# Performance work log

Measured on AMD Instinct MI355X. Metric: run time of the kernel, lower is better.

## Reference

```python
import jax, jax.numpy as jnp
import numpy as np


def setup_inputs() -> dict:
    key = jax.random.key(0)
    k1, k2, k3, k4 = jax.random.split(key, 4)
    B, T, M, Din, Dout = 32, 24, 512, 64, 64
    x = jax.random.normal(k1, (B, T, M, Din), dtype=jnp.float32)
    adj = jax.random.uniform(k2, (M, M), dtype=jnp.float32)
    adj = adj / jnp.sum(adj, axis=-1, keepdims=True)  # row-normalized adjacency
    route_weights = jax.random.normal(k3, (M, Din, Dout), dtype=jnp.float32) * 0.05
    route_bias = jax.random.normal(k4, (M, 1, Dout), dtype=jnp.float32) * 0.05
    return {"x": x, "adj": adj, "route_weights": route_weights, "route_bias": route_bias}


def reference(x, adj, route_weights, route_bias):
    B, T, M, _ = x.shape
    xf = x.reshape(B * T, M, -1)                      # [BT, M, Din]
    # shared adjacency applied across all B*T graphs: one contraction instead of
    # a broadcast bmm
    h = jnp.einsum('mn,bnd->bmd', adj, xf)            # [BT, M, Din]
    # per-node (per-route) weight transform + per-route bias
    h = jnp.einsum('bmd,mdl->bml', h, route_weights)  # [BT, M, Dout]
    h = h + route_bias[:, 0, :][None, :, :]           # bias per route m
    return h.reshape(B, T, M, -1)
```

## Files before the change

kernel.cpp:

```cpp
#include <hip/hip_runtime.h>
#include <stdint.h>

typedef short bf16x8 __attribute__((ext_vector_type(8)));
typedef unsigned short u16x8 __attribute__((ext_vector_type(8)));
typedef float f32x4 __attribute__((ext_vector_type(4)));
typedef float f32x8 __attribute__((ext_vector_type(8)));

constexpr int BT_TOT = 768;
constexpr int M_N    = 512;
constexpr int DD     = 64;
constexpr int WROW   = 72;

__device__ __forceinline__ unsigned short f2bf(float f) {
  unsigned u = __builtin_bit_cast(unsigned, f);
  u += 0x7fffu + ((u >> 16) & 1u);
  return (unsigned short)(u >> 16);
}
__device__ __forceinline__ unsigned pk2(float a, float b) {
  return (unsigned)f2bf(a) | ((unsigned)f2bf(b) << 16);
}

__global__ __launch_bounds__(256)
void prep_adj(const float* __restrict__ adjg, unsigned short* __restrict__ wsadj) {
  int i = (blockIdx.x * 256 + threadIdx.x) * 8;
  f32x8 a = *(const f32x8*)(adjg + i);
  u16x8 r;
  #pragma unroll
  for (int j = 0; j < 8; ++j) r[j] = f2bf(a[j]);
  *(u16x8*)(wsadj + i) = r;
}

template<bool WS>
__global__ __launch_bounds__(512, 2)
void gconv_h(const float* __restrict__ xg,
             const float* __restrict__ adjf,
             const unsigned short* __restrict__ adjb,
             char* __restrict__ hout)
{
  __shared__ char lds[2][32768];

  const int wid  = blockIdx.x;
  const int xcd  = wid & 7;
  const int slot = wid >> 3;
  const int mb   = slot & 3;
  const int btg  = xcd + 8 * (slot >> 2);
  const int bt0  = btg * 2;

  const int tid  = threadIdx.x;
  const int lane = tid & 63;
  const int wv   = tid >> 6;
  const int l15  = lane & 15;
  const int gg   = lane >> 4;
  const int c4   = lane & 15;
  const int wb   = wv & 1;
  const int wm   = wv >> 1;

  const int mlo  = tid >> 3;
  const int oct  = (tid & 7) ^ (mlo & 7);

  f32x4 xv[4];
  u16x8 ab[2];
  f32x8 af_[2];

  auto load_adj = [&](int c) {
    const size_t e0 = (size_t)(mb*128 + mlo     ) * M_N + c*64 + oct*8;
    const size_t e1 = (size_t)(mb*128 + mlo + 64) * M_N + c*64 + oct*8;
    if (WS) { ab[0] = *(const u16x8*)(adjb + e0); ab[1] = *(const u16x8*)(adjb + e1); }
    else    { af_[0] = *(const f32x8*)(adjf + e0); af_[1] = *(const f32x8*)(adjf + e1); }
  };
  auto load_x = [&](int c) {
    #pragma unroll
    for (int s = 0; s < 4; ++s) {
      const int n4 = s*4 + wm;
      xv[s] = *(const f32x4*)(xg + ((size_t)(bt0 + wb) * M_N + c*64 + n4*4 + gg) * DD + c4*4);
    }
  };
  auto write_stage = [&](int c) {
    char* buf = &lds[c & 1][0];
    if (WS) {
      *(u16x8*)(buf + tid*16)        = ab[0];
      *(u16x8*)(buf + 8192 + tid*16) = ab[1];
    } else {
      u16x8 r0, r1;
      #pragma unroll
      for (int j = 0; j < 8; ++j) { r0[j] = f2bf(af_[0][j]); r1[j] = f2bf(af_[1][j]); }
      *(u16x8*)(buf + tid*16)        = r0;
      *(u16x8*)(buf + 8192 + tid*16) = r1;
    }
    char* xt = buf + 16384 + wb*8192;
    const int d = c4*4 + gg;
    #pragma unroll
    for (int s = 0; s < 4; ++s) {
      const int n4 = s*4 + wm;
      unsigned u0 = pk2(xv[s].x, xv[s].y);
      unsigned u1 = pk2(xv[s].z, xv[s].w);
      unsigned t0 = __shfl_xor(u0, 32);
      unsigned t1 = __shfl_xor(u1, 32);
      unsigned v0 = (gg & 2) ? t1 : u0;
      unsigned v1 = (gg & 2) ? u1 : t0;
      unsigned s0 = __shfl_xor(v0, 16);
      unsigned s1 = __shfl_xor(v1, 16);
      unsigned F0 = (gg & 1) ? ((s0 >> 16) | (v0 & 0xFFFF0000u))
                             : ((v0 & 0xFFFFu) | (s0 << 16));
      unsigned F1 = (gg & 1) ? ((s1 >> 16) | (v1 & 0xFFFF0000u))
                             : ((v1 & 0xFFFFu) | (s1 << 16));
      uint2 o2; o2.x = F0; o2.y = F1;
      *(uint2*)(xt + d*128 + (((n4 >> 1) ^ (d & 7)) * 16) + (n4 & 1)*8) = o2;
    }
  };

  f32x4 acc[2][4];
  #pragma unroll
  for (int mt = 0; mt < 2; ++mt)
    #pragma unroll
    for (int dt = 0; dt < 4; ++dt) acc[mt][dt] = f32x4{0.f,0.f,0.f,0.f};

  load_adj(0); load_x(0);

  #pragma unroll 2
  for (int c = 0; c < 8; ++c) {
    write_stage(c);
    __syncthreads();
    if (c < 7) { load_adj(c+1); load_x(c+1); }
    {
      const char* buf  = &lds[c & 1][0];
      const char* adjL = buf;
      const char* xt   = buf + 16384 + wb*8192;
      #pragma unroll
      for (int kl = 0; kl < 2; ++kl) {
        const int sw = ((kl*4 + gg) ^ (l15 & 7)) * 16;
        bf16x8 afr[2], bfx[4];
        #pragma unroll
        for (int mt = 0; mt < 2; ++mt)
          afr[mt] = __builtin_bit_cast(bf16x8,
              *(const u16x8*)(adjL + (wm*32 + mt*16 + l15)*128 + sw));
        #pragma unroll
        for (int dt = 0; dt < 4; ++dt)
          bfx[dt] = __builtin_bit_cast(bf16x8,
              *(const u16x8*)(xt + (dt*16 + l15)*128 + sw));
        #pragma unroll
        for (int mt = 0; mt < 2; ++mt)
          #pragma unroll
          for (int dt = 0; dt < 4; ++dt)
            acc[mt][dt] = __builtin_amdgcn_mfma_f32_16x16x32_bf16(afr[mt], bfx[dt],
                                                                  acc[mt][dt], 0,0,0);
      }
    }
  }

  const int bt = bt0 + wb;
  #pragma unroll
  for (int mt = 0; mt < 2; ++mt)
    #pragma unroll
    for (int dt = 0; dt < 4; ++dt)
      #pragma unroll
      for (int r = 0; r < 4; ++r) {
        int m = mb*128 + wm*32 + mt*16 + gg*4 + r;
        int d = dt*16 + l15;
        *(unsigned short*)(hout + ((size_t)bt*M_N + m)*256 + 2*d)
            = f2bf(acc[mt][dt][r]);
      }
}

__global__ __launch_bounds__(256, 4)
void route_mm(const char* __restrict__ hin,
              const float* __restrict__ wgt,
              const float* __restrict__ bias,
              float* __restrict__ outg)
{
  __shared__ unsigned short wb[128 * WROW];

  const int m0    = blockIdx.x * 2;
  const int btblk = blockIdx.y * 64;
  const int tid   = threadIdx.x;
  const int lane  = tid & 63;
  const int wv    = tid >> 6;
  const int l15   = lane & 15;
  const int gg    = lane >> 4;
  const int dp    = tid & 31;
  const int lo    = tid >> 5;

  { const float* q = wgt + ((size_t)m0*64 + dp*2)*64 + lo*8;
    f32x8 w0 = *(const f32x8*)q;          f32x8 w1 = *(const f32x8*)(q+64);
    f32x8 w2 = *(const f32x8*)(q+4096);   f32x8 w3 = *(const f32x8*)(q+4160);
    #pragma unroll
    for (int e = 0; e < 8; ++e) {
      int lrow = lo*8 + e;
      unsigned v0 = pk2(w0[e], w1[e]);
      unsigned v1 = pk2(w2[e], w3[e]);
      *(unsigned*)(wb + lrow*WROW + dp*2)        = v0;
      *(unsigned*)(wb + (64 + lrow)*WROW + dp*2) = v1;
    }
  }
  __syncthreads();

  const int btw0 = btblk + wv*16;

  #pragma unroll
  for (int mm = 0; mm < 2; ++mm) {
    const int m = m0 + mm;
    bf16x8 afr[2];
    #pragma unroll
    for (int ks = 0; ks < 2; ++ks) {
      const char* hp = hin + ((size_t)(btw0 + l15)*M_N + m)*256 + ks*64 + gg*16;
      afr[ks] = __builtin_bit_cast(bf16x8, *(const u16x8*)hp);
    }
    f32x4 acc[4];
    #pragma unroll
    for (int lt = 0; lt < 4; ++lt) acc[lt] = f32x4{0.f,0.f,0.f,0.f};
    #pragma unroll
    for (int lt = 0; lt < 4; ++lt)
      #pragma unroll
      for (int ks = 0; ks < 2; ++ks) {
        bf16x8 bfr = __builtin_bit_cast(bf16x8,
            *(const u16x8*)(wb + (mm*64 + lt*16 + l15)*WROW + ks*32 + gg*8));
        acc[lt] = __builtin_amdgcn_mfma_f32_16x16x32_bf16(afr[ks], bfr, acc[lt], 0,0,0);
      }
    #pragma unroll
    for (int lt = 0; lt < 4; ++lt) {
      float bv = bias[m*64 + lt*16 + l15];
      #pragma unroll
      for (int r = 0; r < 4; ++r) {
        size_t row = (size_t)(btw0 + gg*4 + r)*M_N + m;
        outg[row*64 + lt*16 + l15] = acc[lt][r] + bv;
      }
    }
  }
}

extern "C" void kernel_launch(void* const* d_in, const int* in_sizes, int n_in,
                              void* d_out, int out_size, void* d_ws, size_t ws_size,
                              hipStream_t stream) {
  const float* xg   = (const float*)d_in[0];
  const float* adjg = (const float*)d_in[1];
  const float* wgt  = (const float*)d_in[2];
  const float* bg   = (const float*)d_in[3];

  const size_t adj_bf_bytes = (size_t)M_N * M_N * 2;
  if (ws_size >= adj_bf_bytes) {
    unsigned short* wsadj = (unsigned short*)d_ws;
    prep_adj<<<dim3(M_N * M_N / (256 * 8)), dim3(256), 0, stream>>>(adjg, wsadj);
    gconv_h<true><<<dim3(1536), dim3(512), 0, stream>>>(
        xg, adjg, wsadj, (char*)d_out);
  } else {
    gconv_h<false><<<dim3(1536), dim3(512), 0, stream>>>(
        xg, adjg, nullptr, (char*)d_out);
  }
  route_mm<<<dim3(M_N/2, BT_TOT/64), dim3(256), 0, stream>>>(
      (const char*)d_out, wgt, bg, (float*)d_out);
}
```

Measured before the change: 99.45 us.

## Load adjacency fragments directly from global and shrink gconv blocks to one BT

The graph-conv kernel no longer stages adjacency tiles in shared memory. Each wave loads its bf16 A-fragments straight from global memory (the bf16 copy is expected to stay in L2), and only the x tile is double-buffered in LDS. Blocks now handle a single bt with 256 threads, so twice as many blocks launch and each uses less LDS, which allows more blocks per CU. The trade-off is that adjacency is no longer shared through LDS across the two bt slices, so global/L2 traffic for it doubles, and its load latency is exposed inside the loop.

```diff
diff --git a/kernel.cpp b/kernel.cpp
--- a/kernel.cpp
+++ b/kernel.cpp
@@ -31,67 +31,43 @@
 }
 
 template<bool WS>
-__global__ __launch_bounds__(512, 2)
+__global__ __launch_bounds__(256, 4)
 void gconv_h(const float* __restrict__ xg,
              const float* __restrict__ adjf,
              const unsigned short* __restrict__ adjb,
              char* __restrict__ hout)
 {
-  __shared__ char lds[2][32768];
+  __shared__ __align__(16) char xlds[2][8192];
 
   const int wid  = blockIdx.x;
   const int xcd  = wid & 7;
   const int slot = wid >> 3;
   const int mb   = slot & 3;
-  const int btg  = xcd + 8 * (slot >> 2);
-  const int bt0  = btg * 2;
+  const int bt   = (slot >> 2) * 8 + xcd;
 
   const int tid  = threadIdx.x;
   const int lane = tid & 63;
   const int wv   = tid >> 6;
   const int l15  = lane & 15;
   const int gg   = lane >> 4;
-  const int c4   = lane & 15;
-  const int wb   = wv & 1;
-  const int wm   = wv >> 1;
-
-  const int mlo  = tid >> 3;
-  const int oct  = (tid & 7) ^ (mlo & 7);
+  const int c4   = l15;
+
+  const float* xsrc = xg + (size_t)bt * (M_N * DD);
 
   f32x4 xv[4];
-  u16x8 ab[2];
-  f32x8 af_[2];
-
-  auto load_adj = [&](int c) {
-    const size_t e0 = (size_t)(mb*128 + mlo     ) * M_N + c*64 + oct*8;
-    const size_t e1 = (size_t)(mb*128 + mlo + 64) * M_N + c*64 + oct*8;
-    if (WS) { ab[0] = *(const u16x8*)(adjb + e0); ab[1] = *(const u16x8*)(adjb + e1); }
-    else    { af_[0] = *(const f32x8*)(adjf + e0); af_[1] = *(const f32x8*)(adjf + e1); }
+  auto load_x = [&](int c) {
+    #pragma unroll
+    for (int s = 0; s < 4; ++s) {
+      const int n4 = s*4 + wv;
+      xv[s] = *(const f32x4*)(xsrc + (size_t)(c*64 + n4*4 + gg) * DD + c4*4);
+    }
   };
-  auto load_x = [&](int c) {
+  auto write_x = [&](int c) {
+    char* xt = &xlds[c & 1][0];
+    const int d = c4*4 + gg;
     #pragma unroll
     for (int s = 0; s < 4; ++s) {
-      const int n4 = s*4 + wm;
-      xv[s] = *(const f32x4*)(xg + ((size_t)(bt0 + wb) * M_N + c*64 + n4*4 + gg) * DD + c4*4);
-    }
-  };
-  auto write_stage = [&](int c) {
-    char* buf = &lds[c & 1][0];
-    if (WS) {
-      *(u16x8*)(buf + tid*16)        = ab[0];
-      *(u16x8*)(buf + 8192 + tid*16) = ab[1];
-    } else {
-      u16x8 r0, r1;
-      #pragma unroll
-      for (int j = 0; j < 8; ++j) { r0[j] = f2bf(af_[0][j]); r1[j] = f2bf(af_[1][j]); }
-      *(u16x8*)(buf + tid*16)        = r0;
-      *(u16x8*)(buf + 8192 + tid*16) = r1;
-    }
-    char* xt = buf + 16384 + wb*8192;
-    const int d = c4*4 + gg;
-    #pragma unroll
-    for (int s = 0; s < 4; ++s) {
-      const int n4 = s*4 + wm;
+      const int n4 = s*4 + wv;
       unsigned u0 = pk2(xv[s].x, xv[s].y);
       unsigned u1 = pk2(xv[s].z, xv[s].w);
       unsigned t0 = __shfl_xor(u0, 32);
@@ -115,47 +91,63 @@
     #pragma unroll
     for (int dt = 0; dt < 4; ++dt) acc[mt][dt] = f32x4{0.f,0.f,0.f,0.f};
 
-  load_adj(0); load_x(0);
-
-  #pragma unroll 2
+  load_x(0);
+  write_x(0);
+  __syncthreads();
+
+  #pragma unroll
   for (int c = 0; c < 8; ++c) {
-    write_stage(c);
-    __syncthreads();
-    if (c < 7) { load_adj(c+1); load_x(c+1); }
-    {
-      const char* buf  = &lds[c & 1][0];
-      const char* adjL = buf;
-      const char* xt   = buf + 16384 + wb*8192;
-      #pragma unroll
-      for (int kl = 0; kl < 2; ++kl) {
-        const int sw = ((kl*4 + gg) ^ (l15 & 7)) * 16;
-        bf16x8 afr[2], bfx[4];
+    u16x8 afr[2][2];
+    if (WS) {
+      #pragma unroll
+      for (int kl = 0; kl < 2; ++kl)
         #pragma unroll
-        for (int mt = 0; mt < 2; ++mt)
-          afr[mt] = __builtin_bit_cast(bf16x8,
-              *(const u16x8*)(adjL + (wm*32 + mt*16 + l15)*128 + sw));
+        for (int mt = 0; mt < 2; ++mt) {
+          const int m = mb*128 + wv*32 + mt*16 + l15;
+          afr[kl][mt] = *(const u16x8*)(adjb + (size_t)m*M_N + c*64 + kl*32 + gg*8);
+        }
+    } else {
+      #pragma unroll
+      for (int kl = 0; kl < 2; ++kl)
+        #pragma unroll
+        for (int mt = 0; mt < 2; ++mt) {
+          const int m = mb*128 + wv*32 + mt*16 + l15;
+          f32x8 a = *(const f32x8*)(adjf + (size_t)m*M_N + c*64 + kl*32 + gg*8);
+          u16x8 r;
+          #pragma unroll
+          for (int j = 0; j < 8; ++j) r[j] = f2bf(a[j]);
+          afr[kl][mt] = r;
+        }
+    }
+
+    if (c < 7) load_x(c + 1);
+
+    const char* xt = &xlds[c & 1][0];
+    #pragma unroll
+    for (int kl = 0; kl < 2; ++kl) {
+      bf16x8 bfx[4];
+      #pragma unroll
+      for (int dt = 0; dt < 4; ++dt)
+        bfx[dt] = __builtin_bit_cast(bf16x8,
+            *(const u16x8*)(xt + (dt*16 + l15)*128 + ((kl*4 + gg) ^ (l15 & 7))*16));
+      #pragma unroll
+      for (int mt = 0; mt < 2; ++mt)
         #pragma unroll
         for (int dt = 0; dt < 4; ++dt)
-          bfx[dt] = __builtin_bit_cast(bf16x8,
-              *(const u16x8*)(xt + (dt*16 + l15)*128 + sw));
-        #pragma unroll
-        for (int mt = 0; mt < 2; ++mt)
-          #pragma unroll
-          for (int dt = 0; dt < 4; ++dt)
-            acc[mt][dt] = __builtin_amdgcn_mfma_f32_16x16x32_bf16(afr[mt], bfx[dt],
-                                                                  acc[mt][dt], 0,0,0);
-      }
-    }
-  }
-
-  const int bt = bt0 + wb;
+          acc[mt][dt] = __builtin_amdgcn_mfma_f32_16x16x32_bf16(
+              __builtin_bit_cast(bf16x8, afr[kl][mt]), bfx[dt], acc[mt][dt], 0,0,0);
+    }
+
+    if (c < 7) { write_x(c + 1); __syncthreads(); }
+  }
+
   #pragma unroll
   for (int mt = 0; mt < 2; ++mt)
     #pragma unroll
     for (int dt = 0; dt < 4; ++dt)
       #pragma unroll
       for (int r = 0; r < 4; ++r) {
-        int m = mb*128 + wm*32 + mt*16 + gg*4 + r;
+        int m = mb*128 + wv*32 + mt*16 + gg*4 + r;
         int d = dt*16 + l15;
         *(unsigned short*)(hout + ((size_t)bt*M_N + m)*256 + 2*d)
             = f2bf(acc[mt][dt][r]);
@@ -240,10 +232,10 @@
   if (ws_size >= adj_bf_bytes) {
     unsigned short* wsadj = (unsigned short*)d_ws;
     prep_adj<<<dim3(M_N * M_N / (256 * 8)), dim3(256), 0, stream>>>(adjg, wsadj);
-    gconv_h<true><<<dim3(1536), dim3(512), 0, stream>>>(
+    gconv_h<true><<<dim3(3072), dim3(256), 0, stream>>>(
         xg, adjg, wsadj, (char*)d_out);
   } else {
-    gconv_h<false><<<dim3(1536), dim3(512), 0, stream>>>(
+    gconv_h<false><<<dim3(3072), dim3(256), 0, stream>>>(
         xg, adjg, nullptr, (char*)d_out);
   }
   route_mm<<<dim3(M_N/2, BT_TOT/64), dim3(256), 0, stream>>>(
```

Result: slower. 107.2 us (+7.8%).
